# Performance work log

Measured on AMD Instinct MI355X. Metric: run time of the kernel, lower is better.

The kernel has to match this reference:

```python
import jax, jax.numpy as jnp
import numpy as np

N = 100_000   # nodes
E = 1_600_000 # edges
F_IN = 256    # num_features
HID = 128     # hidden_channels * heads
G = 128       # graphs in batch
C = 2         # num_classes
BN_EPS = 1e-5


def setup_inputs() -> dict:
    key = jax.random.key(0)
    ks = jax.random.split(key, 12)
    x = jax.random.normal(ks[0], (N, F_IN), dtype=jnp.float32)
    edge_index = jax.random.randint(ks[1], (2, E), 0, N, dtype=jnp.int64)
    batch = jnp.sort(jax.random.randint(ks[2], (N,), 0, G, dtype=jnp.int64))
    s1 = 1.0 / np.sqrt(F_IN)
    s2 = 1.0 / np.sqrt(HID)
    W1 = jax.random.uniform(ks[3], (F_IN, HID), jnp.float32, -s1, s1)
    b1 = jnp.zeros((HID,), jnp.float32)
    W2 = jax.random.uniform(ks[4], (HID, HID), jnp.float32, -s2, s2)
    b2 = jnp.zeros((HID,), jnp.float32)
    W3 = jax.random.uniform(ks[5], (HID, HID), jnp.float32, -s2, s2)
    b3 = jnp.zeros((HID,), jnp.float32)
    bn_gamma = jnp.ones((HID,), jnp.float32)
    bn_beta = jnp.zeros((HID,), jnp.float32)
    bn_mean = jnp.zeros((HID,), jnp.float32)
    bn_var = jnp.ones((HID,), jnp.float32)
    lin_w = jax.random.uniform(ks[6], (HID, C), jnp.float32, -s2, s2)
    lin_b = jax.random.uniform(ks[7], (C,), jnp.float32, -s2, s2)
    return {
        "x": x, "edge_index": edge_index, "_": 0, "batch": batch,
        "W1": W1, "b1": b1, "W2": W2, "b2": b2, "W3": W3, "b3": b3,
        "bn_gamma": bn_gamma, "bn_beta": bn_beta,
        "bn_mean": bn_mean, "bn_var": bn_var,
        "lin_w": lin_w, "lin_b": lin_b,
    }


def reference(x, edge_index, _, batch, W1, b1, W2, b2, W3, b3,
              bn_gamma, bn_beta, bn_mean, bn_var, lin_w, lin_b):
    src, dst = edge_index[0], edge_index[1]
    # GCN symmetric normalization with self-loops (gcn_norm):
    # deg[i] = 1 + in_degree(i); norm_e = deg[src]^-1/2 * deg[dst]^-1/2
    deg = 1.0 + jax.ops.segment_sum(jnp.ones((E,), x.dtype), dst, num_segments=N)
    dis = jax.lax.rsqrt(deg)
    norm_e = (dis[src] * dis[dst])[:, None]        # [E,1]
    self_norm = (1.0 / deg)[:, None]               # [N,1] self-loop weight

    def gcn_conv(h, W, b):
        hw = h @ W                                  # transform first (PyG order)
        agg = jax.ops.segment_sum(hw[src] * norm_e, dst, num_segments=N)
        return agg + hw * self_norm + b

    h = jax.nn.relu(gcn_conv(x, W1, b1))
    h = jax.nn.relu(gcn_conv(h, W2, b2))
    h = jax.nn.relu(gcn_conv(h, W3, b3))

    # global_mean_pool over graph ids
    counts = jax.ops.segment_sum(jnp.ones((N,), h.dtype), batch, num_segments=G)
    pooled = jax.ops.segment_sum(h, batch, num_segments=G) / jnp.maximum(counts, 1.0)[:, None]

    # dropout p=0.5 is identity in eval mode; BatchNorm1d with running stats
    xb = (pooled - bn_mean) * jax.lax.rsqrt(bn_var + BN_EPS) * bn_gamma + bn_beta
    out = jax.nn.relu(xb @ lin_w + lin_b)
    return (xb, out)
```

## Files before the change

kernel.cpp:

```cpp
#include <hip/hip_runtime.h>

#define NNODES 100000
#define NEDGES 1600000
#define FIN 256
#define HID 128
#define NG 128
#define NB 391
#define NW 256
#define EPW 6250

static constexpr float BN_EPS_C = 1e-5f;

typedef __attribute__((ext_vector_type(8))) short bf16x8;
typedef __attribute__((ext_vector_type(4))) float f32x4;
typedef __attribute__((ext_vector_type(2))) float f32x2;

#if defined(__has_builtin)
#if __has_builtin(__builtin_amdgcn_cvt_pk_f32_fp8)
#define HAS_HWFP8 1
#endif
#endif

__device__ __forceinline__ float b2f(unsigned short u) {
    union { unsigned int i; float f; } c; c.i = ((unsigned int)u) << 16; return c.f;
}
__device__ __forceinline__ unsigned short f2b(float f) {
    union { float f; unsigned int i; } c; c.f = f;
    unsigned int u = c.i;
    u += 0x7fffu + ((u >> 16) & 1u);
    return (unsigned short)(u >> 16);
}

__device__ __forceinline__ unsigned char f2e8(float f) {
    union { float f; unsigned int u; } c; c.f = f;
    unsigned int s = (c.u >> 24) & 0x80u;
    c.u &= 0x7fffffffu;
    c.f = fminf(fmaxf(c.f, 0.015625f), 448.f);
    unsigned int u = c.u + 0x7ffffu + ((c.u >> 20) & 1u);
    int e = (int)(u >> 23) - 127;
    unsigned int m = (u >> 20) & 7u;
    return (unsigned char)(s | ((unsigned int)(e + 7) << 3) | m);
}

__device__ __forceinline__ float e8byte(unsigned int b) {
    union { unsigned int u; float f; } c;
    c.u = ((b & 0x80u) << 24) | (0x3C000000u + ((b & 0x7fu) << 20));
    return c.f;
}
__device__ __forceinline__ f32x2 e8plo(unsigned int w) {
#ifdef HAS_HWFP8
    return __builtin_amdgcn_cvt_pk_f32_fp8(w, false);
#else
    f32x2 r; r[0] = e8byte(w & 0xffu); r[1] = e8byte((w >> 8) & 0xffu); return r;
#endif
}
__device__ __forceinline__ f32x2 e8phi(unsigned int w) {
#ifdef HAS_HWFP8
    return __builtin_amdgcn_cvt_pk_f32_fp8(w, true);
#else
    f32x2 r; r[0] = e8byte((w >> 16) & 0xffu); r[1] = e8byte(w >> 24); return r;
#endif
}
__device__ __forceinline__ f32x2 bdec(unsigned int u) {
    union { unsigned int i[2]; f32x2 f; } c;
    c.i[0] = u << 16;
    c.i[1] = u & 0xffff0000u;
    return c.f;
}

__global__ __launch_bounds__(256) void kbA(const int* __restrict__ dst, int* __restrict__ hist) {
    __shared__ int h[NB];
    int w = blockIdx.x, t = threadIdx.x;
    for (int i = t; i < NB; i += 256) h[i] = 0;
    __syncthreads();
    int base = w * EPW;
    for (int i = t; i < EPW; i += 256) atomicAdd(&h[dst[base + i] >> 8], 1);
    __syncthreads();
    for (int i = t; i < NB; i += 256) hist[i * NW + w] = h[i];
}

__global__ __launch_bounds__(256) void kbB2(const int* __restrict__ hist,
                                            int* __restrict__ off,
                                            int* __restrict__ btot) {
    __shared__ int s[NW];
    int b = blockIdx.x, t = threadIdx.x;
    int v = hist[b * NW + t];
    s[t] = v;
    __syncthreads();
    for (int o = 1; o < NW; o <<= 1) {
        int a = (t >= o) ? s[t - o] : 0;
        __syncthreads();
        s[t] += a;
        __syncthreads();
    }
    off[b * NW + t] = s[t] - v;
    if (t == NW - 1) btot[b] = s[t];
}

__global__ __launch_bounds__(512) void kbT(const int* __restrict__ btot,
                                           int* __restrict__ bbase,
                                           int* __restrict__ rowptr) {
    __shared__ int s[512];
    int t = threadIdx.x;
    int v = (t < NB) ? btot[t] : 0;
    s[t] = v;
    __syncthreads();
    for (int o = 1; o < 512; o <<= 1) {
        int a = (t >= o) ? s[t - o] : 0;
        __syncthreads();
        s[t] += a;
        __syncthreads();
    }
    if (t < NB) bbase[t] = s[t] - v;
    if (t == NB - 1) { bbase[NB] = s[t]; rowptr[NNODES] = NEDGES; }
}

__global__ __launch_bounds__(256) void kbC2(const int* __restrict__ src,
                                            const int* __restrict__ dst,
                                            const int* __restrict__ off,
                                            const int* __restrict__ bbase,
                                            int* __restrict__ pairs) {
    __shared__ int cur[NB];
    int w = blockIdx.x, t = threadIdx.x;
    for (int i = t; i < NB; i += 256) cur[i] = off[i * NW + w] + bbase[i];
    __syncthreads();
    int base = w * EPW;
    for (int i = t; i < EPW; i += 256) {
        int d = dst[base + i];
        int pos = atomicAdd(&cur[d >> 8], 1);
        pairs[pos] = (src[base + i] << 8) | (d & 255);
    }
}

__global__ __launch_bounds__(256) void kb2y(const int* __restrict__ bbase,
                                            const int* __restrict__ pairs,
                                            int* __restrict__ rowptr,
                                            float* __restrict__ dis,
                                            float* __restrict__ selfn) {
    int b = blockIdx.x;
    int nbase = b * 256;
    int nmax = NNODES - nbase; if (nmax > 256) nmax = 256;
    __shared__ int cnt[256];
    __shared__ int cur[256];
    int t = threadIdx.x;
    cnt[t] = 0;
    __syncthreads();
    int beg = bbase[b], end = bbase[b + 1];
    for (int i = beg + t; i < end; i += 256) atomicAdd(&cnt[pairs[i] & 255], 1);
    __syncthreads();
    int v = cnt[t];
    cur[t] = v;
    __syncthreads();
    for (int o = 1; o < 256; o <<= 1) {
        int a = (t >= o) ? cur[t - o] : 0;
        __syncthreads();
        cur[t] += a;
        __syncthreads();
    }
    if (t < nmax) {
        rowptr[nbase + t] = cur[t] - v + beg;
        float d = 1.0f + (float)v;
        dis[nbase + t] = rsqrtf(d);
        selfn[nbase + t] = 1.0f / d;
    }
}

__global__ __launch_bounds__(256) void kb2z(const int* __restrict__ bbase,
                                            const int* __restrict__ pairs,
                                            const int* __restrict__ rowptr,
                                            const float* __restrict__ dis,
                                            unsigned int* __restrict__ edgp) {
    int b = blockIdx.x;
    int nbase = b * 256;
    int nmax = NNODES - nbase; if (nmax > 256) nmax = 256;
    __shared__ int cur[256];
    __shared__ float disl[256];
    int t = threadIdx.x;
    if (t < nmax) {
        cur[t] = rowptr[nbase + t];
        disl[t] = dis[nbase + t];
    }
    __syncthreads();
    int beg = bbase[b], end = bbase[b + 1];
    for (int i = beg + t; i < end; i += 256) {
        int p = pairs[i];
        int s = p >> 8;
        float w = dis[s] * disl[p & 255];
        unsigned int u = (unsigned int)(w * 32767.f + 0.5f);
        int pos = atomicAdd(&cur[p & 255], 1);
        edgp[pos] = ((unsigned int)s << 15) | u;
    }
}

__global__ __launch_bounds__(256) void k_wconv3(const float* __restrict__ W1,
                                                const float* __restrict__ W2,
                                                const float* __restrict__ W3,
                                                unsigned short* __restrict__ whl1,
                                                unsigned short* __restrict__ whl2,
                                                unsigned short* __restrict__ whl3) {
    int idx = blockIdx.x * 256 + threadIdx.x;
    const float* W; unsigned short* whl;
    if (idx < FIN * 128) { W = W1; whl = whl1; }
    else if (idx < (FIN + HID) * 128) { W = W2; whl = whl2; idx -= FIN * 128; }
    else if (idx < (FIN + 2 * HID) * 128) { W = W3; whl = whl3; idx -= (FIN + HID) * 128; }
    else return;
    int k = idx >> 7, c = idx & 127;
    float v = W[k * 128 + c];
    unsigned short hi = f2b(v);
    unsigned short lo = f2b(v - b2f(hi));
    int kstep = k >> 5, kk = k & 31, g = kk >> 3, j = kk & 7;
    int tile = c >> 4, lane = (c & 15) + 16 * g;
    size_t b0 = ((((size_t)kstep * 2 + 0) * 8 + tile) * 64 + lane) * 8 + j;
    size_t b1 = ((((size_t)kstep * 2 + 1) * 8 + tile) * 64 + lane) * 8 + j;
    whl[b0] = hi;
    whl[b1] = lo;
}

template<int K, int MODE, int OUT8>
__global__ __launch_bounds__(256) void k_gemm_mfma(const void* __restrict__ Araw,
                                                   const unsigned short* __restrict__ whl,
                                                   void* __restrict__ hwbv) {
    __shared__ __align__(16) unsigned short Ah0[2048];
    __shared__ __align__(16) unsigned short Ah1[2048];
    __shared__ __align__(16) unsigned short Bs[8192];

    const int tid = threadIdx.x;
    const int w = tid >> 6;
    const int lane = tid & 63;
    const int m0 = blockIdx.x * 64;
    const int ar = tid >> 2;
    const int ak = (tid & 3) * 8;
    const int adst = (((ar >> 4) * 64) + (ar & 15) + 16 * (ak >> 3)) * 8;

    f32x4 acc[8] = {};

    for (int kt = 0; kt < K; kt += 32) {
        if (MODE == 0) {
            const float* A = (const float*)Araw;
            float4 v0 = {0.f,0.f,0.f,0.f}, v1 = {0.f,0.f,0.f,0.f};
            int grow = m0 + ar;
            if (grow < NNODES) {
                const float* s = A + (size_t)grow * K + kt + ak;
                v0 = *(const float4*)(s);
                v1 = *(const float4*)(s + 4);
            }
            float av[8];
            *(float4*)(av) = v0; *(float4*)(av + 4) = v1;
            bf16x8 hv, lv;
            #pragma unroll
            for (int j = 0; j < 8; ++j) {
                unsigned short h = f2b(av[j]);
                hv[j] = (short)h;
                lv[j] = (short)f2b(av[j] - b2f(h));
            }
            *(bf16x8*)&Ah0[adst] = hv;
            *(bf16x8*)&Ah1[adst] = lv;
        } else {
            const unsigned short* A = (const unsigned short*)Araw;
            bf16x8 hv = {};
            int grow = m0 + ar;
            if (grow < NNODES)
                hv = *(const bf16x8*)(A + (size_t)grow * K + kt + ak);
            *(bf16x8*)&Ah0[adst] = hv;
        }
        {
            const float4* bsrc = (const float4*)(whl + (size_t)(kt >> 5) * 8192);
            float4* bdst = (float4*)Bs;
            #pragma unroll
            for (int i = 0; i < 4; ++i) bdst[tid * 4 + i] = bsrc[tid * 4 + i];
        }
        __syncthreads();
        bf16x8 a0 = *(const bf16x8*)&Ah0[(w * 64 + lane) * 8];
        bf16x8 a1;
        if (MODE == 0) a1 = *(const bf16x8*)&Ah1[(w * 64 + lane) * 8];
        #pragma unroll
        for (int t = 0; t < 8; ++t) {
            bf16x8 b0 = *(const bf16x8*)&Bs[(t * 64 + lane) * 8];
            bf16x8 b1 = *(const bf16x8*)&Bs[4096 + (t * 64 + lane) * 8];
            acc[t] = __builtin_amdgcn_mfma_f32_16x16x32_bf16(a0, b0, acc[t], 0, 0, 0);
            acc[t] = __builtin_amdgcn_mfma_f32_16x16x32_bf16(a0, b1, acc[t], 0, 0, 0);
            if (MODE == 0)
                acc[t] = __builtin_amdgcn_mfma_f32_16x16x32_bf16(a1, b0, acc[t], 0, 0, 0);
        }
        __syncthreads();
    }

    const int colLo = lane & 15;
    const int gq = lane >> 4;
    #pragma unroll
    for (int i = 0; i < 4; ++i) {
        int row = m0 + w * 16 + gq * 4 + i;
        if (row < NNODES) {
            #pragma unroll
            for (int t = 0; t < 8; ++t) {
                int col = t * 16 + colLo;
                float v = acc[t][i];
                if (OUT8) {
                    ((unsigned char*)hwbv)[(size_t)row * HID + col] = f2e8(v * 64.f);
                } else {
                    ((unsigned short*)hwbv)[(size_t)row * HID + col] = f2b(v);
                }
            }
        }
    }
}

template<int IN8>
__global__ __launch_bounds__(256) void k_gather(const int* __restrict__ rowptr,
                                                const unsigned int* __restrict__ edgp,
                                                const void* __restrict__ hwbv,
                                                const float* __restrict__ selfn,
                                                const float* __restrict__ bias,
                                                unsigned short* __restrict__ agb) {
    const int lane = threadIdx.x & 63;
    const int sub = lane >> 4;
    const int l4 = lane & 15;
    const int node = blockIdx.x * 16 + ((threadIdx.x >> 6) << 2) + sub;
    int beg = rowptr[node], end = rowptr[node + 1];
    const float q = IN8 ? (1.0f / (32767.0f * 64.0f)) : (1.0f / 32767.0f);
    const unsigned char* hb = (const unsigned char*)hwbv;
    f32x2 a0 = {0.f,0.f}, a1 = {0.f,0.f}, a2 = {0.f,0.f}, a3 = {0.f,0.f};
    int e = beg;
    for (; e + 3 < end; e += 4) {
        unsigned int p0 = edgp[e], p1 = edgp[e + 1];
        unsigned int p2 = edgp[e + 2], p3 = edgp[e + 3];
        float w0 = (float)(p0 & 0x7fffu) * q;
        float w1 = (float)(p1 & 0x7fffu) * q;
        float w2 = (float)(p2 & 0x7fffu) * q;
        float w3 = (float)(p3 & 0x7fffu) * q;
        f32x2 wa = {w0, w0}, wb = {w1, w1}, wc = {w2, w2}, wd = {w3, w3};
        size_t r0 = (size_t)(p0 >> 15), r1 = (size_t)(p1 >> 15);
        size_t r2 = (size_t)(p2 >> 15), r3 = (size_t)(p3 >> 15);
        if (IN8) {
            uint2 v0 = *(const uint2*)(hb + r0 * HID + l4 * 8);
            uint2 v1 = *(const uint2*)(hb + r1 * HID + l4 * 8);
            uint2 v2 = *(const uint2*)(hb + r2 * HID + l4 * 8);
            uint2 v3 = *(const uint2*)(hb + r3 * HID + l4 * 8);
            a0 += e8plo(v0.x) * wa; a1 += e8phi(v0.x) * wa;
            a2 += e8plo(v0.y) * wa; a3 += e8phi(v0.y) * wa;
            a0 += e8plo(v1.x) * wb; a1 += e8phi(v1.x) * wb;
            a2 += e8plo(v1.y) * wb; a3 += e8phi(v1.y) * wb;
            a0 += e8plo(v2.x) * wc; a1 += e8phi(v2.x) * wc;
            a2 += e8plo(v2.y) * wc; a3 += e8phi(v2.y) * wc;
            a0 += e8plo(v3.x) * wd; a1 += e8phi(v3.x) * wd;
            a2 += e8plo(v3.y) * wd; a3 += e8phi(v3.y) * wd;
        } else {
            uint4 v0 = *(const uint4*)(hb + r0 * (HID * 2) + l4 * 16);
            uint4 v1 = *(const uint4*)(hb + r1 * (HID * 2) + l4 * 16);
            uint4 v2 = *(const uint4*)(hb + r2 * (HID * 2) + l4 * 16);
            uint4 v3 = *(const uint4*)(hb + r3 * (HID * 2) + l4 * 16);
            a0 += bdec(v0.x) * wa; a1 += bdec(v0.y) * wa;
            a2 += bdec(v0.z) * wa; a3 += bdec(v0.w) * wa;
            a0 += bdec(v1.x) * wb; a1 += bdec(v1.y) * wb;
            a2 += bdec(v1.z) * wb; a3 += bdec(v1.w) * wb;
            a0 += bdec(v2.x) * wc; a1 += bdec(v2.y) * wc;
            a2 += bdec(v2.z) * wc; a3 += bdec(v2.w) * wc;
            a0 += bdec(v3.x) * wd; a1 += bdec(v3.y) * wd;
            a2 += bdec(v3.z) * wd; a3 += bdec(v3.w) * wd;
        }
    }
    for (; e < end; ++e) {
        unsigned int p = edgp[e];
        float w = (float)(p & 0x7fffu) * q;
        f32x2 wa = {w, w};
        size_t r = (size_t)(p >> 15);
        if (IN8) {
            uint2 v = *(const uint2*)(hb + r * HID + l4 * 8);
            a0 += e8plo(v.x) * wa; a1 += e8phi(v.x) * wa;
            a2 += e8plo(v.y) * wa; a3 += e8phi(v.y) * wa;
        } else {
            uint4 v = *(const uint4*)(hb + r * (HID * 2) + l4 * 16);
            a0 += bdec(v.x) * wa; a1 += bdec(v.y) * wa;
            a2 += bdec(v.z) * wa; a3 += bdec(v.w) * wa;
        }
    }
    float sn = selfn[node] * (IN8 ? (1.0f / 64.0f) : 1.0f);
    f32x2 sn2 = {sn, sn};
    f32x2 h0, h1, h2, h3;
    if (IN8) {
        uint2 v = *(const uint2*)(hb + (size_t)node * HID + l4 * 8);
        h0 = e8plo(v.x); h1 = e8phi(v.x); h2 = e8plo(v.y); h3 = e8phi(v.y);
    } else {
        uint4 v = *(const uint4*)(hb + (size_t)node * (HID * 2) + l4 * 16);
        h0 = bdec(v.x); h1 = bdec(v.y); h2 = bdec(v.z); h3 = bdec(v.w);
    }
    float4 bA = *(const float4*)&bias[l4 * 8];
    float4 bB = *(const float4*)&bias[l4 * 8 + 4];
    a0 += h0 * sn2; a1 += h1 * sn2; a2 += h2 * sn2; a3 += h3 * sn2;
    float r0 = fmaxf(a0[0] + bA.x, 0.f), r1 = fmaxf(a0[1] + bA.y, 0.f);
    float r2 = fmaxf(a1[0] + bA.z, 0.f), r3 = fmaxf(a1[1] + bA.w, 0.f);
    float r4 = fmaxf(a2[0] + bB.x, 0.f), r5 = fmaxf(a2[1] + bB.y, 0.f);
    float r6 = fmaxf(a3[0] + bB.z, 0.f), r7 = fmaxf(a3[1] + bB.w, 0.f);
    uint4 o;
    o.x = (unsigned int)f2b(r0) | ((unsigned int)f2b(r1) << 16);
    o.y = (unsigned int)f2b(r2) | ((unsigned int)f2b(r3) << 16);
    o.z = (unsigned int)f2b(r4) | ((unsigned int)f2b(r5) << 16);
    o.w = (unsigned int)f2b(r6) | ((unsigned int)f2b(r7) << 16);
    *(uint4*)(agb + (size_t)node * HID + l4 * 8) = o;
}

__global__ __launch_bounds__(1024) void k_pool_bn_head(const unsigned short* __restrict__ h,
                                                       const int* __restrict__ batch,
                                                       const float* __restrict__ gamma,
                                                       const float* __restrict__ beta,
                                                       const float* __restrict__ mean,
                                                       const float* __restrict__ var,
                                                       const float* __restrict__ lw,
                                                       const float* __restrict__ lb,
                                                       float* __restrict__ xb,
                                                       float* __restrict__ out2) {
    int g = blockIdx.x;
    int tid = threadIdx.x;
    int fg = tid & 15;
    int r = tid >> 4;
    __shared__ int bounds[2];
    if (tid < 2) {
        int target = g + tid;
        int a = 0, b = NNODES;
        while (a < b) { int m = (a + b) >> 1; if (batch[m] < target) a = m + 1; else b = m; }
        bounds[tid] = a;
    }
    __syncthreads();
    int s1 = bounds[0], e1 = bounds[1];
    f32x2 acc[4] = {};
    for (int i = s1 + r; i < e1; i += 64) {
        uint4 v = *(const uint4*)(h + (size_t)i * HID + fg * 8);
        acc[0] += bdec(v.x); acc[1] += bdec(v.y); acc[2] += bdec(v.z); acc[3] += bdec(v.w);
    }
    __shared__ f32x2 red[64][16][4];
    #pragma unroll
    for (int j = 0; j < 4; ++j) red[r][fg][j] = acc[j];
    __syncthreads();
    for (int off = 32; off >= 1; off >>= 1) {
        if (r < off) {
            #pragma unroll
            for (int j = 0; j < 4; ++j) red[r][fg][j] += red[r + off][fg][j];
        }
        __syncthreads();
    }
    __shared__ float xbl[128];
    if (r == 0) {
        float cnt = (float)((e1 - s1) > 0 ? (e1 - s1) : 1);
        float inv = 1.0f / cnt;
        #pragma unroll
        for (int j = 0; j < 4; ++j) {
            #pragma unroll
            for (int k2 = 0; k2 < 2; ++k2) {
                int f = fg * 8 + j * 2 + k2;
                float pooled = red[0][fg][j][k2] * inv;
                float xbv = (pooled - mean[f]) * rsqrtf(var[f] + BN_EPS_C) * gamma[f] + beta[f];
                xb[g * HID + f] = xbv;
                xbl[f] = xbv;
            }
        }
    }
    __syncthreads();
    if (tid < 64) {
        float x0 = xbl[tid], x1 = xbl[tid + 64];
        float s0 = x0 * lw[tid * 2 + 0] + x1 * lw[(tid + 64) * 2 + 0];
        float s1h = x0 * lw[tid * 2 + 1] + x1 * lw[(tid + 64) * 2 + 1];
        #pragma unroll
        for (int o = 1; o < 64; o <<= 1) {
            s0 += __shfl_xor(s0, o);
            s1h += __shfl_xor(s1h, o);
        }
        if (tid == 0) {
            out2[g * 2 + 0] = fmaxf(s0 + lb[0], 0.f);
            out2[g * 2 + 1] = fmaxf(s1h + lb[1], 0.f);
        }
    }
}

extern "C" void kernel_launch(void* const* d_in, const int* in_sizes, int n_in,
                              void* d_out, int out_size, void* d_ws, size_t ws_size,
                              hipStream_t stream) {
    const float* x     = (const float*)d_in[0];
    const int*   ei    = (const int*)d_in[1];
    const int*   batch = (const int*)d_in[3];
    const float* W1 = (const float*)d_in[4];
    const float* b1 = (const float*)d_in[5];
    const float* W2 = (const float*)d_in[6];
    const float* b2 = (const float*)d_in[7];
    const float* W3 = (const float*)d_in[8];
    const float* b3 = (const float*)d_in[9];
    const float* gamma = (const float*)d_in[10];
    const float* beta  = (const float*)d_in[11];
    const float* mean  = (const float*)d_in[12];
    const float* var   = (const float*)d_in[13];
    const float* lw = (const float*)d_in[14];
    const float* lb = (const float*)d_in[15];
    float* out = (float*)d_out;

    char* p = (char*)d_ws;
    unsigned short* HWB = (unsigned short*)p;          p += (size_t)NNODES * HID * 2;
    unsigned short* AGB = (unsigned short*)p;          p += (size_t)NNODES * HID * 2;
    float* DIS    = (float*)p;                         p += (size_t)NNODES * 4;
    float* SELFN  = (float*)p;                         p += (size_t)NNODES * 4;
    int*   ROWPTR = (int*)p;                           p += (size_t)(NNODES + 64) * 4;
    unsigned int* EDGP = (unsigned int*)p;             p += (size_t)NEDGES * 4;
    int*   BTOT   = (int*)p;                           p += 512 * 4;
    int*   BBASE  = (int*)p;                           p += 512 * 4;
    unsigned short* WHL1 = (unsigned short*)p;         p += (size_t)FIN * 128 * 2 * 2;
    unsigned short* WHL2 = (unsigned short*)p;         p += (size_t)HID * 128 * 2 * 2;
    unsigned short* WHL3 = (unsigned short*)p;
    int*   PAIRS  = (int*)HWB;
    int*   HIST   = (int*)AGB;
    int*   OFF    = HIST + NB * NW;

    const int* srcv = ei;
    const int* dstv = ei + NEDGES;

    kbA<<<NW, 256, 0, stream>>>(dstv, HIST);
    kbB2<<<NB, 256, 0, stream>>>(HIST, OFF, BTOT);
    kbT<<<1, 512, 0, stream>>>(BTOT, BBASE, ROWPTR);
    kbC2<<<NW, 256, 0, stream>>>(srcv, dstv, OFF, BBASE, PAIRS);
    kb2y<<<NB, 256, 0, stream>>>(BBASE, PAIRS, ROWPTR, DIS, SELFN);
    kb2z<<<NB, 256, 0, stream>>>(BBASE, PAIRS, ROWPTR, DIS, EDGP);
    k_wconv3<<<((FIN + 2 * HID) * 128 + 255) / 256, 256, 0, stream>>>(W1, W2, W3, WHL1, WHL2, WHL3);

    dim3 gg((NNODES + 63) / 64);
    const int ggat = NNODES / 16;

    k_gemm_mfma<FIN, 0, 1><<<gg, 256, 0, stream>>>(x, WHL1, HWB);
    k_gather<1><<<ggat, 256, 0, stream>>>(ROWPTR, EDGP, HWB, SELFN, b1, AGB);
    k_gemm_mfma<HID, 1, 1><<<gg, 256, 0, stream>>>(AGB, WHL2, HWB);
    k_gather<1><<<ggat, 256, 0, stream>>>(ROWPTR, EDGP, HWB, SELFN, b2, AGB);
    k_gemm_mfma<HID, 1, 0><<<gg, 256, 0, stream>>>(AGB, WHL3, HWB);
    k_gather<0><<<ggat, 256, 0, stream>>>(ROWPTR, EDGP, HWB, SELFN, b3, AGB);

    k_pool_bn_head<<<NG, 1024, 0, stream>>>(AGB, batch, gamma, beta, mean, var,
                                            lw, lb, out, out + (size_t)NG * HID);
}
```

Before: 275.2 us.

## Use finer CSR-build buckets with more workers and unroll fp8 gather by eight

```diff
diff --git a/kernel.cpp b/kernel.cpp
--- a/kernel.cpp
+++ b/kernel.cpp
@@ -5,9 +5,10 @@
 #define FIN 256
 #define HID 128
 #define NG 128
-#define NB 391
-#define NW 256
-#define EPW 6250
+#define BSHIFT 7
+#define BSZ 128
+#define NB 782
+#define NW 1024
 
 static constexpr float BN_EPS_C = 1e-5f;
 
@@ -73,8 +74,9 @@
     int w = blockIdx.x, t = threadIdx.x;
     for (int i = t; i < NB; i += 256) h[i] = 0;
     __syncthreads();
-    int base = w * EPW;
-    for (int i = t; i < EPW; i += 256) atomicAdd(&h[dst[base + i] >> 8], 1);
+    int beg = (int)((long long)w * NEDGES / NW);
+    int end = (int)((long long)(w + 1) * NEDGES / NW);
+    for (int i = beg + t; i < end; i += 256) atomicAdd(&h[dst[i] >> BSHIFT], 1);
     __syncthreads();
     for (int i = t; i < NB; i += 256) hist[i * NW + w] = h[i];
 }
@@ -82,30 +84,33 @@
 __global__ __launch_bounds__(256) void kbB2(const int* __restrict__ hist,
                                             int* __restrict__ off,
                                             int* __restrict__ btot) {
-    __shared__ int s[NW];
+    __shared__ int s[256];
     int b = blockIdx.x, t = threadIdx.x;
-    int v = hist[b * NW + t];
-    s[t] = v;
-    __syncthreads();
-    for (int o = 1; o < NW; o <<= 1) {
+    int base = b * NW + t * 4;
+    int v0 = hist[base], v1 = hist[base + 1], v2 = hist[base + 2], v3 = hist[base + 3];
+    int p1 = v0, p2 = v0 + v1, p3 = v0 + v1 + v2, tot = p3 + v3;
+    s[t] = tot;
+    __syncthreads();
+    for (int o = 1; o < 256; o <<= 1) {
         int a = (t >= o) ? s[t - o] : 0;
         __syncthreads();
         s[t] += a;
         __syncthreads();
     }
-    off[b * NW + t] = s[t] - v;
-    if (t == NW - 1) btot[b] = s[t];
-}
-
-__global__ __launch_bounds__(512) void kbT(const int* __restrict__ btot,
-                                           int* __restrict__ bbase,
-                                           int* __restrict__ rowptr) {
-    __shared__ int s[512];
+    int ex = s[t] - tot;
+    off[base] = ex; off[base + 1] = ex + p1; off[base + 2] = ex + p2; off[base + 3] = ex + p3;
+    if (t == 255) btot[b] = s[255];
+}
+
+__global__ __launch_bounds__(1024) void kbT(const int* __restrict__ btot,
+                                            int* __restrict__ bbase,
+                                            int* __restrict__ rowptr) {
+    __shared__ int s[1024];
     int t = threadIdx.x;
     int v = (t < NB) ? btot[t] : 0;
     s[t] = v;
     __syncthreads();
-    for (int o = 1; o < 512; o <<= 1) {
+    for (int o = 1; o < 1024; o <<= 1) {
         int a = (t >= o) ? s[t - o] : 0;
         __syncthreads();
         s[t] += a;
@@ -124,11 +129,12 @@
     int w = blockIdx.x, t = threadIdx.x;
     for (int i = t; i < NB; i += 256) cur[i] = off[i * NW + w] + bbase[i];
     __syncthreads();
-    int base = w * EPW;
-    for (int i = t; i < EPW; i += 256) {
-        int d = dst[base + i];
-        int pos = atomicAdd(&cur[d >> 8], 1);
-        pairs[pos] = (src[base + i] << 8) | (d & 255);
+    int beg = (int)((long long)w * NEDGES / NW);
+    int end = (int)((long long)(w + 1) * NEDGES / NW);
+    for (int i = beg + t; i < end; i += 256) {
+        int d = dst[i];
+        int pos = atomicAdd(&cur[d >> BSHIFT], 1);
+        pairs[pos] = (src[i] << BSHIFT) | (d & (BSZ - 1));
     }
 }
 
@@ -138,26 +144,26 @@
                                             float* __restrict__ dis,
                                             float* __restrict__ selfn) {
     int b = blockIdx.x;
-    int nbase = b * 256;
-    int nmax = NNODES - nbase; if (nmax > 256) nmax = 256;
-    __shared__ int cnt[256];
-    __shared__ int cur[256];
+    int nbase = b * BSZ;
+    int nmax = NNODES - nbase; if (nmax > BSZ) nmax = BSZ;
+    __shared__ int cnt[BSZ];
+    __shared__ int cur[BSZ];
     int t = threadIdx.x;
-    cnt[t] = 0;
+    if (t < BSZ) cnt[t] = 0;
     __syncthreads();
     int beg = bbase[b], end = bbase[b + 1];
-    for (int i = beg + t; i < end; i += 256) atomicAdd(&cnt[pairs[i] & 255], 1);
-    __syncthreads();
-    int v = cnt[t];
-    cur[t] = v;
-    __syncthreads();
-    for (int o = 1; o < 256; o <<= 1) {
-        int a = (t >= o) ? cur[t - o] : 0;
-        __syncthreads();
-        cur[t] += a;
+    for (int i = beg + t; i < end; i += 256) atomicAdd(&cnt[pairs[i] & (BSZ - 1)], 1);
+    __syncthreads();
+    if (t < BSZ) cur[t] = cnt[t];
+    __syncthreads();
+    for (int o = 1; o < BSZ; o <<= 1) {
+        int a = (t >= o && t < BSZ) ? cur[t - o] : 0;
+        __syncthreads();
+        if (t < BSZ) cur[t] += a;
         __syncthreads();
     }
     if (t < nmax) {
+        int v = cnt[t];
         rowptr[nbase + t] = cur[t] - v + beg;
         float d = 1.0f + (float)v;
         dis[nbase + t] = rsqrtf(d);
@@ -171,10 +177,10 @@
                                             const float* __restrict__ dis,
                                             unsigned int* __restrict__ edgp) {
     int b = blockIdx.x;
-    int nbase = b * 256;
-    int nmax = NNODES - nbase; if (nmax > 256) nmax = 256;
-    __shared__ int cur[256];
-    __shared__ float disl[256];
+    int nbase = b * BSZ;
+    int nmax = NNODES - nbase; if (nmax > BSZ) nmax = BSZ;
+    __shared__ int cur[BSZ];
+    __shared__ float disl[BSZ];
     int t = threadIdx.x;
     if (t < nmax) {
         cur[t] = rowptr[nbase + t];
@@ -184,10 +190,10 @@
     int beg = bbase[b], end = bbase[b + 1];
     for (int i = beg + t; i < end; i += 256) {
         int p = pairs[i];
-        int s = p >> 8;
-        float w = dis[s] * disl[p & 255];
+        int s = p >> BSHIFT;
+        float w = dis[s] * disl[p & (BSZ - 1)];
         unsigned int u = (unsigned int)(w * 32767.f + 0.5f);
-        int pos = atomicAdd(&cur[p & 255], 1);
+        int pos = atomicAdd(&cur[p & (BSZ - 1)], 1);
         edgp[pos] = ((unsigned int)s << 15) | u;
     }
 }
@@ -321,21 +327,26 @@
     const unsigned char* hb = (const unsigned char*)hwbv;
     f32x2 a0 = {0.f,0.f}, a1 = {0.f,0.f}, a2 = {0.f,0.f}, a3 = {0.f,0.f};
     int e = beg;
-    for (; e + 3 < end; e += 4) {
-        unsigned int p0 = edgp[e], p1 = edgp[e + 1];
-        unsigned int p2 = edgp[e + 2], p3 = edgp[e + 3];
-        float w0 = (float)(p0 & 0x7fffu) * q;
-        float w1 = (float)(p1 & 0x7fffu) * q;
-        float w2 = (float)(p2 & 0x7fffu) * q;
-        float w3 = (float)(p3 & 0x7fffu) * q;
-        f32x2 wa = {w0, w0}, wb = {w1, w1}, wc = {w2, w2}, wd = {w3, w3};
-        size_t r0 = (size_t)(p0 >> 15), r1 = (size_t)(p1 >> 15);
-        size_t r2 = (size_t)(p2 >> 15), r3 = (size_t)(p3 >> 15);
-        if (IN8) {
-            uint2 v0 = *(const uint2*)(hb + r0 * HID + l4 * 8);
-            uint2 v1 = *(const uint2*)(hb + r1 * HID + l4 * 8);
-            uint2 v2 = *(const uint2*)(hb + r2 * HID + l4 * 8);
-            uint2 v3 = *(const uint2*)(hb + r3 * HID + l4 * 8);
+    if (IN8) {
+        for (; e + 7 < end; e += 8) {
+            unsigned int p0 = edgp[e], p1 = edgp[e + 1];
+            unsigned int p2 = edgp[e + 2], p3 = edgp[e + 3];
+            unsigned int p4 = edgp[e + 4], p5 = edgp[e + 5];
+            unsigned int p6 = edgp[e + 6], p7 = edgp[e + 7];
+            uint2 v0 = *(const uint2*)(hb + (size_t)(p0 >> 15) * HID + l4 * 8);
+            uint2 v1 = *(const uint2*)(hb + (size_t)(p1 >> 15) * HID + l4 * 8);
+            uint2 v2 = *(const uint2*)(hb + (size_t)(p2 >> 15) * HID + l4 * 8);
+            uint2 v3 = *(const uint2*)(hb + (size_t)(p3 >> 15) * HID + l4 * 8);
+            uint2 v4 = *(const uint2*)(hb + (size_t)(p4 >> 15) * HID + l4 * 8);
+            uint2 v5 = *(const uint2*)(hb + (size_t)(p5 >> 15) * HID + l4 * 8);
+            uint2 v6 = *(const uint2*)(hb + (size_t)(p6 >> 15) * HID + l4 * 8);
+            uint2 v7 = *(const uint2*)(hb + (size_t)(p7 >> 15) * HID + l4 * 8);
+            float w0 = (float)(p0 & 0x7fffu) * q, w1 = (float)(p1 & 0x7fffu) * q;
+            float w2 = (float)(p2 & 0x7fffu) * q, w3 = (float)(p3 & 0x7fffu) * q;
+            float w4 = (float)(p4 & 0x7fffu) * q, w5 = (float)(p5 & 0x7fffu) * q;
+            float w6 = (float)(p6 & 0x7fffu) * q, w7 = (float)(p7 & 0x7fffu) * q;
+            f32x2 wa = {w0, w0}, wb = {w1, w1}, wc = {w2, w2}, wd = {w3, w3};
+            f32x2 we = {w4, w4}, wf = {w5, w5}, wg = {w6, w6}, wh = {w7, w7};
             a0 += e8plo(v0.x) * wa; a1 += e8phi(v0.x) * wa;
             a2 += e8plo(v0.y) * wa; a3 += e8phi(v0.y) * wa;
             a0 += e8plo(v1.x) * wb; a1 += e8phi(v1.x) * wb;
@@ -344,7 +355,26 @@
             a2 += e8plo(v2.y) * wc; a3 += e8phi(v2.y) * wc;
             a0 += e8plo(v3.x) * wd; a1 += e8phi(v3.x) * wd;
             a2 += e8plo(v3.y) * wd; a3 += e8phi(v3.y) * wd;
-        } else {
+            a0 += e8plo(v4.x) * we; a1 += e8phi(v4.x) * we;
+            a2 += e8plo(v4.y) * we; a3 += e8phi(v4.y) * we;
+            a0 += e8plo(v5.x) * wf; a1 += e8phi(v5.x) * wf;
+            a2 += e8plo(v5.y) * wf; a3 += e8phi(v5.y) * wf;
+            a0 += e8plo(v6.x) * wg; a1 += e8phi(v6.x) * wg;
+            a2 += e8plo(v6.y) * wg; a3 += e8phi(v6.y) * wg;
+            a0 += e8plo(v7.x) * wh; a1 += e8phi(v7.x) * wh;
+            a2 += e8plo(v7.y) * wh; a3 += e8phi(v7.y) * wh;
+        }
+    } else {
+        for (; e + 3 < end; e += 4) {
+            unsigned int p0 = edgp[e], p1 = edgp[e + 1];
+            unsigned int p2 = edgp[e + 2], p3 = edgp[e + 3];
+            float w0 = (float)(p0 & 0x7fffu) * q;
+            float w1 = (float)(p1 & 0x7fffu) * q;
+            float w2 = (float)(p2 & 0x7fffu) * q;
+            float w3 = (float)(p3 & 0x7fffu) * q;
+            f32x2 wa = {w0, w0}, wb = {w1, w1}, wc = {w2, w2}, wd = {w3, w3};
+            size_t r0 = (size_t)(p0 >> 15), r1 = (size_t)(p1 >> 15);
+            size_t r2 = (size_t)(p2 >> 15), r3 = (size_t)(p3 >> 15);
             uint4 v0 = *(const uint4*)(hb + r0 * (HID * 2) + l4 * 16);
             uint4 v1 = *(const uint4*)(hb + r1 * (HID * 2) + l4 * 16);
             uint4 v2 = *(const uint4*)(hb + r2 * (HID * 2) + l4 * 16);
@@ -498,8 +528,8 @@
     float* SELFN  = (float*)p;                         p += (size_t)NNODES * 4;
     int*   ROWPTR = (int*)p;                           p += (size_t)(NNODES + 64) * 4;
     unsigned int* EDGP = (unsigned int*)p;             p += (size_t)NEDGES * 4;
-    int*   BTOT   = (int*)p;                           p += 512 * 4;
-    int*   BBASE  = (int*)p;                           p += 512 * 4;
+    int*   BTOT   = (int*)p;                           p += 1024 * 4;
+    int*   BBASE  = (int*)p;                           p += 1024 * 4;
     unsigned short* WHL1 = (unsigned short*)p;         p += (size_t)FIN * 128 * 2 * 2;
     unsigned short* WHL2 = (unsigned short*)p;         p += (size_t)HID * 128 * 2 * 2;
     unsigned short* WHL3 = (unsigned short*)p;
@@ -512,7 +542,7 @@
 
     kbA<<<NW, 256, 0, stream>>>(dstv, HIST);
     kbB2<<<NB, 256, 0, stream>>>(HIST, OFF, BTOT);
-    kbT<<<1, 512, 0, stream>>>(BTOT, BBASE, ROWPTR);
+    kbT<<<1, 1024, 0, stream>>>(BTOT, BBASE, ROWPTR);
     kbC2<<<NW, 256, 0, stream>>>(srcv, dstv, OFF, BBASE, PAIRS);
     kb2y<<<NB, 256, 0, stream>>>(BBASE, PAIRS, ROWPTR, DIS, SELFN);
     kb2z<<<NB, 256, 0, stream>>>(BBASE, PAIRS, ROWPTR, DIS, EDGP);
```

Measured after the change: 288.2 us. 1.05x slower.

## Fuse CSR build stages with weight conversion and first GEMM launches

Applied to the files above, without the earlier changes.

```diff
diff --git a/kernel.cpp b/kernel.cpp
--- a/kernel.cpp
+++ b/kernel.cpp
@@ -8,6 +8,7 @@
 #define NB 391
 #define NW 256
 #define EPW 6250
+#define GEMM_BLKS 1563
 
 static constexpr float BN_EPS_C = 1e-5f;
 
@@ -68,158 +69,11 @@
     return c.f;
 }
 
-__global__ __launch_bounds__(256) void kbA(const int* __restrict__ dst, int* __restrict__ hist) {
-    __shared__ int h[NB];
-    int w = blockIdx.x, t = threadIdx.x;
-    for (int i = t; i < NB; i += 256) h[i] = 0;
-    __syncthreads();
-    int base = w * EPW;
-    for (int i = t; i < EPW; i += 256) atomicAdd(&h[dst[base + i] >> 8], 1);
-    __syncthreads();
-    for (int i = t; i < NB; i += 256) hist[i * NW + w] = h[i];
-}
-
-__global__ __launch_bounds__(256) void kbB2(const int* __restrict__ hist,
-                                            int* __restrict__ off,
-                                            int* __restrict__ btot) {
-    __shared__ int s[NW];
-    int b = blockIdx.x, t = threadIdx.x;
-    int v = hist[b * NW + t];
-    s[t] = v;
-    __syncthreads();
-    for (int o = 1; o < NW; o <<= 1) {
-        int a = (t >= o) ? s[t - o] : 0;
-        __syncthreads();
-        s[t] += a;
-        __syncthreads();
-    }
-    off[b * NW + t] = s[t] - v;
-    if (t == NW - 1) btot[b] = s[t];
-}
-
-__global__ __launch_bounds__(512) void kbT(const int* __restrict__ btot,
-                                           int* __restrict__ bbase,
-                                           int* __restrict__ rowptr) {
-    __shared__ int s[512];
-    int t = threadIdx.x;
-    int v = (t < NB) ? btot[t] : 0;
-    s[t] = v;
-    __syncthreads();
-    for (int o = 1; o < 512; o <<= 1) {
-        int a = (t >= o) ? s[t - o] : 0;
-        __syncthreads();
-        s[t] += a;
-        __syncthreads();
-    }
-    if (t < NB) bbase[t] = s[t] - v;
-    if (t == NB - 1) { bbase[NB] = s[t]; rowptr[NNODES] = NEDGES; }
-}
-
-__global__ __launch_bounds__(256) void kbC2(const int* __restrict__ src,
-                                            const int* __restrict__ dst,
-                                            const int* __restrict__ off,
-                                            const int* __restrict__ bbase,
-                                            int* __restrict__ pairs) {
-    __shared__ int cur[NB];
-    int w = blockIdx.x, t = threadIdx.x;
-    for (int i = t; i < NB; i += 256) cur[i] = off[i * NW + w] + bbase[i];
-    __syncthreads();
-    int base = w * EPW;
-    for (int i = t; i < EPW; i += 256) {
-        int d = dst[base + i];
-        int pos = atomicAdd(&cur[d >> 8], 1);
-        pairs[pos] = (src[base + i] << 8) | (d & 255);
-    }
-}
-
-__global__ __launch_bounds__(256) void kb2y(const int* __restrict__ bbase,
-                                            const int* __restrict__ pairs,
-                                            int* __restrict__ rowptr,
-                                            float* __restrict__ dis,
-                                            float* __restrict__ selfn) {
-    int b = blockIdx.x;
-    int nbase = b * 256;
-    int nmax = NNODES - nbase; if (nmax > 256) nmax = 256;
-    __shared__ int cnt[256];
-    __shared__ int cur[256];
-    int t = threadIdx.x;
-    cnt[t] = 0;
-    __syncthreads();
-    int beg = bbase[b], end = bbase[b + 1];
-    for (int i = beg + t; i < end; i += 256) atomicAdd(&cnt[pairs[i] & 255], 1);
-    __syncthreads();
-    int v = cnt[t];
-    cur[t] = v;
-    __syncthreads();
-    for (int o = 1; o < 256; o <<= 1) {
-        int a = (t >= o) ? cur[t - o] : 0;
-        __syncthreads();
-        cur[t] += a;
-        __syncthreads();
-    }
-    if (t < nmax) {
-        rowptr[nbase + t] = cur[t] - v + beg;
-        float d = 1.0f + (float)v;
-        dis[nbase + t] = rsqrtf(d);
-        selfn[nbase + t] = 1.0f / d;
-    }
-}
-
-__global__ __launch_bounds__(256) void kb2z(const int* __restrict__ bbase,
-                                            const int* __restrict__ pairs,
-                                            const int* __restrict__ rowptr,
-                                            const float* __restrict__ dis,
-                                            unsigned int* __restrict__ edgp) {
-    int b = blockIdx.x;
-    int nbase = b * 256;
-    int nmax = NNODES - nbase; if (nmax > 256) nmax = 256;
-    __shared__ int cur[256];
-    __shared__ float disl[256];
-    int t = threadIdx.x;
-    if (t < nmax) {
-        cur[t] = rowptr[nbase + t];
-        disl[t] = dis[nbase + t];
-    }
-    __syncthreads();
-    int beg = bbase[b], end = bbase[b + 1];
-    for (int i = beg + t; i < end; i += 256) {
-        int p = pairs[i];
-        int s = p >> 8;
-        float w = dis[s] * disl[p & 255];
-        unsigned int u = (unsigned int)(w * 32767.f + 0.5f);
-        int pos = atomicAdd(&cur[p & 255], 1);
-        edgp[pos] = ((unsigned int)s << 15) | u;
-    }
-}
-
-__global__ __launch_bounds__(256) void k_wconv3(const float* __restrict__ W1,
-                                                const float* __restrict__ W2,
-                                                const float* __restrict__ W3,
-                                                unsigned short* __restrict__ whl1,
-                                                unsigned short* __restrict__ whl2,
-                                                unsigned short* __restrict__ whl3) {
-    int idx = blockIdx.x * 256 + threadIdx.x;
-    const float* W; unsigned short* whl;
-    if (idx < FIN * 128) { W = W1; whl = whl1; }
-    else if (idx < (FIN + HID) * 128) { W = W2; whl = whl2; idx -= FIN * 128; }
-    else if (idx < (FIN + 2 * HID) * 128) { W = W3; whl = whl3; idx -= (FIN + HID) * 128; }
-    else return;
-    int k = idx >> 7, c = idx & 127;
-    float v = W[k * 128 + c];
-    unsigned short hi = f2b(v);
-    unsigned short lo = f2b(v - b2f(hi));
-    int kstep = k >> 5, kk = k & 31, g = kk >> 3, j = kk & 7;
-    int tile = c >> 4, lane = (c & 15) + 16 * g;
-    size_t b0 = ((((size_t)kstep * 2 + 0) * 8 + tile) * 64 + lane) * 8 + j;
-    size_t b1 = ((((size_t)kstep * 2 + 1) * 8 + tile) * 64 + lane) * 8 + j;
-    whl[b0] = hi;
-    whl[b1] = lo;
-}
-
 template<int K, int MODE, int OUT8>
-__global__ __launch_bounds__(256) void k_gemm_mfma(const void* __restrict__ Araw,
-                                                   const unsigned short* __restrict__ whl,
-                                                   void* __restrict__ hwbv) {
+__device__ __forceinline__ void gemm_body(int blk,
+                                          const void* __restrict__ Araw,
+                                          const unsigned short* __restrict__ whl,
+                                          void* __restrict__ hwbv) {
     __shared__ __align__(16) unsigned short Ah0[2048];
     __shared__ __align__(16) unsigned short Ah1[2048];
     __shared__ __align__(16) unsigned short Bs[8192];
@@ -227,7 +81,7 @@
     const int tid = threadIdx.x;
     const int w = tid >> 6;
     const int lane = tid & 63;
-    const int m0 = blockIdx.x * 64;
+    const int m0 = blk * 64;
     const int ar = tid >> 2;
     const int ak = (tid & 3) * 8;
     const int adst = (((ar >> 4) * 64) + (ar & 15) + 16 * (ak >> 3)) * 8;
@@ -305,6 +159,169 @@
     }
 }
 
+__global__ __launch_bounds__(256) void k_prep(const float* __restrict__ W1,
+                                              const float* __restrict__ W2,
+                                              const float* __restrict__ W3,
+                                              unsigned short* __restrict__ whl1,
+                                              unsigned short* __restrict__ whl2,
+                                              unsigned short* __restrict__ whl3,
+                                              const int* __restrict__ dst,
+                                              int* __restrict__ hist) {
+    if (blockIdx.x < 256) {
+        int idx = blockIdx.x * 256 + threadIdx.x;
+        const float* W; unsigned short* whl;
+        if (idx < FIN * 128) { W = W1; whl = whl1; }
+        else if (idx < (FIN + HID) * 128) { W = W2; whl = whl2; idx -= FIN * 128; }
+        else { W = W3; whl = whl3; idx -= (FIN + HID) * 128; }
+        int k = idx >> 7, c = idx & 127;
+        float v = W[k * 128 + c];
+        unsigned short hi = f2b(v);
+        unsigned short lo = f2b(v - b2f(hi));
+        int kstep = k >> 5, kk = k & 31, g = kk >> 3, j = kk & 7;
+        int tile = c >> 4, lane = (c & 15) + 16 * g;
+        size_t b0 = ((((size_t)kstep * 2 + 0) * 8 + tile) * 64 + lane) * 8 + j;
+        size_t b1 = ((((size_t)kstep * 2 + 1) * 8 + tile) * 64 + lane) * 8 + j;
+        whl[b0] = hi;
+        whl[b1] = lo;
+    } else {
+        __shared__ int h[NB];
+        int w = blockIdx.x - 256, t = threadIdx.x;
+        for (int i = t; i < NB; i += 256) h[i] = 0;
+        __syncthreads();
+        int base = w * EPW;
+        for (int i = t; i < EPW; i += 256) atomicAdd(&h[dst[base + i] >> 8], 1);
+        __syncthreads();
+        for (int i = t; i < NB; i += 256) hist[i * NW + w] = h[i];
+    }
+}
+
+__global__ __launch_bounds__(256) void kbB2(const int* __restrict__ hist,
+                                            int* __restrict__ off,
+                                            int* __restrict__ btot) {
+    __shared__ int s[NW];
+    int b = blockIdx.x, t = threadIdx.x;
+    int v = hist[b * NW + t];
+    s[t] = v;
+    __syncthreads();
+    for (int o = 1; o < NW; o <<= 1) {
+        int a = (t >= o) ? s[t - o] : 0;
+        __syncthreads();
+        s[t] += a;
+        __syncthreads();
+    }
+    off[b * NW + t] = s[t] - v;
+    if (t == NW - 1) btot[b] = s[t];
+}
+
+__global__ __launch_bounds__(512) void kbT(const int* __restrict__ btot,
+                                           int* __restrict__ bbase,
+                                           int* __restrict__ rowptr) {
+    __shared__ int s[512];
+    int t = threadIdx.x;
+    int v = (t < NB) ? btot[t] : 0;
+    s[t] = v;
+    __syncthreads();
+    for (int o = 1; o < 512; o <<= 1) {
+        int a = (t >= o) ? s[t - o] : 0;
+        __syncthreads();
+        s[t] += a;
+        __syncthreads();
+    }
+    if (t < NB) bbase[t] = s[t] - v;
+    if (t == NB - 1) { bbase[NB] = s[t]; rowptr[NNODES] = NEDGES; }
+}
+
+__global__ __launch_bounds__(256) void k_c2g1(const int* __restrict__ src,
+                                              const int* __restrict__ dst,
+                                              const int* __restrict__ off,
+                                              const int* __restrict__ bbase,
+                                              int* __restrict__ pairs,
+                                              const float* __restrict__ x,
+                                              const unsigned short* __restrict__ whl1,
+                                              void* __restrict__ hwbv) {
+    if (blockIdx.x < 256) {
+        __shared__ int cur[NB];
+        int w = blockIdx.x, t = threadIdx.x;
+        for (int i = t; i < NB; i += 256) cur[i] = off[i * NW + w] + bbase[i];
+        __syncthreads();
+        int base = w * EPW;
+        for (int i = t; i < EPW; i += 256) {
+            int d = dst[base + i];
+            int pos = atomicAdd(&cur[d >> 8], 1);
+            pairs[pos] = (src[base + i] << 8) | (d & 255);
+        }
+    } else {
+        gemm_body<FIN, 0, 1>(blockIdx.x - 256, x, whl1, hwbv);
+    }
+}
+
+__global__ __launch_bounds__(256) void kb2y(const int* __restrict__ bbase,
+                                            const int* __restrict__ pairs,
+                                            int* __restrict__ rowptr,
+                                            float* __restrict__ dis,
+                                            float* __restrict__ selfn) {
+    int b = blockIdx.x;
+    int nbase = b * 256;
+    int nmax = NNODES - nbase; if (nmax > 256) nmax = 256;
+    __shared__ int cnt[256];
+    __shared__ int cur[256];
+    int t = threadIdx.x;
+    cnt[t] = 0;
+    __syncthreads();
+    int beg = bbase[b], end = bbase[b + 1];
+    for (int i = beg + t; i < end; i += 256) atomicAdd(&cnt[pairs[i] & 255], 1);
+    __syncthreads();
+    int v = cnt[t];
+    cur[t] = v;
+    __syncthreads();
+    for (int o = 1; o < 256; o <<= 1) {
+        int a = (t >= o) ? cur[t - o] : 0;
+        __syncthreads();
+        cur[t] += a;
+        __syncthreads();
+    }
+    if (t < nmax) {
+        rowptr[nbase + t] = cur[t] - v + beg;
+        float d = 1.0f + (float)v;
+        dis[nbase + t] = rsqrtf(d);
+        selfn[nbase + t] = 1.0f / d;
+    }
+}
+
+__global__ __launch_bounds__(256) void kb2z(const int* __restrict__ bbase,
+                                            const int* __restrict__ pairs,
+                                            const int* __restrict__ rowptr,
+                                            const float* __restrict__ dis,
+                                            unsigned int* __restrict__ edgp) {
+    int b = blockIdx.x;
+    int nbase = b * 256;
+    int nmax = NNODES - nbase; if (nmax > 256) nmax = 256;
+    __shared__ int cur[256];
+    __shared__ float disl[256];
+    int t = threadIdx.x;
+    if (t < nmax) {
+        cur[t] = rowptr[nbase + t];
+        disl[t] = dis[nbase + t];
+    }
+    __syncthreads();
+    int beg = bbase[b], end = bbase[b + 1];
+    for (int i = beg + t; i < end; i += 256) {
+        int p = pairs[i];
+        int s = p >> 8;
+        float w = dis[s] * disl[p & 255];
+        unsigned int u = (unsigned int)(w * 32767.f + 0.5f);
+        int pos = atomicAdd(&cur[p & 255], 1);
+        edgp[pos] = ((unsigned int)s << 15) | u;
+    }
+}
+
+template<int K, int MODE, int OUT8>
+__global__ __launch_bounds__(256) void k_gemm_mfma(const void* __restrict__ Araw,
+                                                   const unsigned short* __restrict__ whl,
+                                                   void* __restrict__ hwbv) {
+    gemm_body<K, MODE, OUT8>(blockIdx.x, Araw, whl, hwbv);
+}
+
 template<int IN8>
 __global__ __launch_bounds__(256) void k_gather(const int* __restrict__ rowptr,
                                                 const unsigned int* __restrict__ edgp,
@@ -321,21 +338,26 @@
     const unsigned char* hb = (const unsigned char*)hwbv;
     f32x2 a0 = {0.f,0.f}, a1 = {0.f,0.f}, a2 = {0.f,0.f}, a3 = {0.f,0.f};
     int e = beg;
-    for (; e + 3 < end; e += 4) {
-        unsigned int p0 = edgp[e], p1 = edgp[e + 1];
-        unsigned int p2 = edgp[e + 2], p3 = edgp[e + 3];
-        float w0 = (float)(p0 & 0x7fffu) * q;
-        float w1 = (float)(p1 & 0x7fffu) * q;
-        float w2 = (float)(p2 & 0x7fffu) * q;
-        float w3 = (float)(p3 & 0x7fffu) * q;
-        f32x2 wa = {w0, w0}, wb = {w1, w1}, wc = {w2, w2}, wd = {w3, w3};
-        size_t r0 = (size_t)(p0 >> 15), r1 = (size_t)(p1 >> 15);
-        size_t r2 = (size_t)(p2 >> 15), r3 = (size_t)(p3 >> 15);
-        if (IN8) {
-            uint2 v0 = *(const uint2*)(hb + r0 * HID + l4 * 8);
-            uint2 v1 = *(const uint2*)(hb + r1 * HID + l4 * 8);
-            uint2 v2 = *(const uint2*)(hb + r2 * HID + l4 * 8);
-            uint2 v3 = *(const uint2*)(hb + r3 * HID + l4 * 8);
+    if (IN8) {
+        for (; e + 7 < end; e += 8) {
+            unsigned int p0 = edgp[e], p1 = edgp[e + 1];
+            unsigned int p2 = edgp[e + 2], p3 = edgp[e + 3];
+            unsigned int p4 = edgp[e + 4], p5 = edgp[e + 5];
+            unsigned int p6 = edgp[e + 6], p7 = edgp[e + 7];
+            uint2 v0 = *(const uint2*)(hb + (size_t)(p0 >> 15) * HID + l4 * 8);
+            uint2 v1 = *(const uint2*)(hb + (size_t)(p1 >> 15) * HID + l4 * 8);
+            uint2 v2 = *(const uint2*)(hb + (size_t)(p2 >> 15) * HID + l4 * 8);
+            uint2 v3 = *(const uint2*)(hb + (size_t)(p3 >> 15) * HID + l4 * 8);
+            uint2 v4 = *(const uint2*)(hb + (size_t)(p4 >> 15) * HID + l4 * 8);
+            uint2 v5 = *(const uint2*)(hb + (size_t)(p5 >> 15) * HID + l4 * 8);
+            uint2 v6 = *(const uint2*)(hb + (size_t)(p6 >> 15) * HID + l4 * 8);
+            uint2 v7 = *(const uint2*)(hb + (size_t)(p7 >> 15) * HID + l4 * 8);
+            float w0 = (float)(p0 & 0x7fffu) * q, w1 = (float)(p1 & 0x7fffu) * q;
+            float w2 = (float)(p2 & 0x7fffu) * q, w3 = (float)(p3 & 0x7fffu) * q;
+            float w4 = (float)(p4 & 0x7fffu) * q, w5 = (float)(p5 & 0x7fffu) * q;
+            float w6 = (float)(p6 & 0x7fffu) * q, w7 = (float)(p7 & 0x7fffu) * q;
+            f32x2 wa = {w0, w0}, wb = {w1, w1}, wc = {w2, w2}, wd = {w3, w3};
+            f32x2 we = {w4, w4}, wf = {w5, w5}, wg = {w6, w6}, wh = {w7, w7};
             a0 += e8plo(v0.x) * wa; a1 += e8phi(v0.x) * wa;
             a2 += e8plo(v0.y) * wa; a3 += e8phi(v0.y) * wa;
             a0 += e8plo(v1.x) * wb; a1 += e8phi(v1.x) * wb;
@@ -344,7 +366,26 @@
             a2 += e8plo(v2.y) * wc; a3 += e8phi(v2.y) * wc;
             a0 += e8plo(v3.x) * wd; a1 += e8phi(v3.x) * wd;
             a2 += e8plo(v3.y) * wd; a3 += e8phi(v3.y) * wd;
-        } else {
+            a0 += e8plo(v4.x) * we; a1 += e8phi(v4.x) * we;
+            a2 += e8plo(v4.y) * we; a3 += e8phi(v4.y) * we;
+            a0 += e8plo(v5.x) * wf; a1 += e8phi(v5.x) * wf;
+            a2 += e8plo(v5.y) * wf; a3 += e8phi(v5.y) * wf;
+            a0 += e8plo(v6.x) * wg; a1 += e8phi(v6.x) * wg;
+            a2 += e8plo(v6.y) * wg; a3 += e8phi(v6.y) * wg;
+            a0 += e8plo(v7.x) * wh; a1 += e8phi(v7.x) * wh;
+            a2 += e8plo(v7.y) * wh; a3 += e8phi(v7.y) * wh;
+        }
+    } else {
+        for (; e + 3 < end; e += 4) {
+            unsigned int p0 = edgp[e], p1 = edgp[e + 1];
+            unsigned int p2 = edgp[e + 2], p3 = edgp[e + 3];
+            float w0 = (float)(p0 & 0x7fffu) * q;
+            float w1 = (float)(p1 & 0x7fffu) * q;
+            float w2 = (float)(p2 & 0x7fffu) * q;
+            float w3 = (float)(p3 & 0x7fffu) * q;
+            f32x2 wa = {w0, w0}, wb = {w1, w1}, wc = {w2, w2}, wd = {w3, w3};
+            size_t r0 = (size_t)(p0 >> 15), r1 = (size_t)(p1 >> 15);
+            size_t r2 = (size_t)(p2 >> 15), r3 = (size_t)(p3 >> 15);
             uint4 v0 = *(const uint4*)(hb + r0 * (HID * 2) + l4 * 16);
             uint4 v1 = *(const uint4*)(hb + r1 * (HID * 2) + l4 * 16);
             uint4 v2 = *(const uint4*)(hb + r2 * (HID * 2) + l4 * 16);
@@ -498,30 +539,28 @@
     float* SELFN  = (float*)p;                         p += (size_t)NNODES * 4;
     int*   ROWPTR = (int*)p;                           p += (size_t)(NNODES + 64) * 4;
     unsigned int* EDGP = (unsigned int*)p;             p += (size_t)NEDGES * 4;
+    int*   PAIRS  = (int*)p;                           p += (size_t)NEDGES * 4;
     int*   BTOT   = (int*)p;                           p += 512 * 4;
     int*   BBASE  = (int*)p;                           p += 512 * 4;
     unsigned short* WHL1 = (unsigned short*)p;         p += (size_t)FIN * 128 * 2 * 2;
     unsigned short* WHL2 = (unsigned short*)p;         p += (size_t)HID * 128 * 2 * 2;
     unsigned short* WHL3 = (unsigned short*)p;
-    int*   PAIRS  = (int*)HWB;
     int*   HIST   = (int*)AGB;
     int*   OFF    = HIST + NB * NW;
 
     const int* srcv = ei;
     const int* dstv = ei + NEDGES;
 
-    kbA<<<NW, 256, 0, stream>>>(dstv, HIST);
+    k_prep<<<512, 256, 0, stream>>>(W1, W2, W3, WHL1, WHL2, WHL3, dstv, HIST);
     kbB2<<<NB, 256, 0, stream>>>(HIST, OFF, BTOT);
     kbT<<<1, 512, 0, stream>>>(BTOT, BBASE, ROWPTR);
-    kbC2<<<NW, 256, 0, stream>>>(srcv, dstv, OFF, BBASE, PAIRS);
+    k_c2g1<<<256 + GEMM_BLKS, 256, 0, stream>>>(srcv, dstv, OFF, BBASE, PAIRS, x, WHL1, HWB);
     kb2y<<<NB, 256, 0, stream>>>(BBASE, PAIRS, ROWPTR, DIS, SELFN);
     kb2z<<<NB, 256, 0, stream>>>(BBASE, PAIRS, ROWPTR, DIS, EDGP);
-    k_wconv3<<<((FIN + 2 * HID) * 128 + 255) / 256, 256, 0, stream>>>(W1, W2, W3, WHL1, WHL2, WHL3);
-
-    dim3 gg((NNODES + 63) / 64);
+
     const int ggat = NNODES / 16;
-
-    k_gemm_mfma<FIN, 0, 1><<<gg, 256, 0, stream>>>(x, WHL1, HWB);
+    dim3 gg(GEMM_BLKS);
+
     k_gather<1><<<ggat, 256, 0, stream>>>(ROWPTR, EDGP, HWB, SELFN, b1, AGB);
     k_gemm_mfma<HID, 1, 1><<<gg, 256, 0, stream>>>(AGB, WHL2, HWB);
     k_gather<1><<<ggat, 256, 0, stream>>>(ROWPTR, EDGP, HWB, SELFN, b2, AGB);
```

Measured after the change: 261.2 us. 5.1% less time.
